# Performance work log

Hardware: AMD Instinct MI355X
Metric: run time of the kernel (lower is better)

The kernel has to match this reference:

```python
import jax, jax.numpy as jnp
import numpy as np

B, H, S, DK, DV = 2, 16, 2048, 64, 64


def setup_inputs() -> dict:
    key = jax.random.key(0)
    kq, kk, kv = jax.random.split(key, 3)
    queries = jax.random.normal(kq, (B, H, S, DK), dtype=jnp.float32)
    keys = jax.random.normal(kk, (B, H, S, DK), dtype=jnp.float32)
    values = jax.random.normal(kv, (B, H, S, DV), dtype=jnp.float32)
    # causal boolean mask, broadcastable over batch and heads
    mask = jnp.tril(jnp.ones((S, S), dtype=bool))[None, None, :, :]
    return {"queries": queries, "keys": keys, "values": values, "d_k": DK, "mask": mask}


def reference(queries, keys, values, d_k, mask):
    scale = 1.0 / jnp.sqrt(jnp.float32(d_k))
    # scores: [B, H, S, S]
    scores = jnp.einsum("bhqd,bhkd->bhqk", queries, keys) * scale
    mask_f = mask.astype(jnp.float32)
    scores = scores + (-1e9) * (1.0 - mask_f)
    weights = jax.nn.softmax(scores, axis=-1)
    # second mask step from the original: min(|mask|, |weights|)
    weights = jnp.minimum(jnp.abs(mask_f), jnp.abs(weights))
    return jnp.einsum("bhqk,bhkd->bhqd", weights, values)
```

## Files before the change

kernel.cpp:

```cpp
#include <hip/hip_runtime.h>
#include <hip/hip_bf16.h>

#define B_ 2
#define H_ 16
#define S_ 2048
#define D_ 64

typedef __attribute__((ext_vector_type(8))) short bf16x8;
typedef __attribute__((ext_vector_type(8))) unsigned short u16x8;
typedef __attribute__((ext_vector_type(4))) unsigned int u32x4;
typedef __attribute__((ext_vector_type(4))) float f32x4;
typedef unsigned short ushort_t;

#define SCALE 0.18033688011112042f
#define MFIX 12.0f

__device__ __forceinline__ unsigned short f2bf(float x) {
  unsigned int u = __builtin_bit_cast(unsigned int, x);
  unsigned int r = (u + 0x7FFFu + ((u >> 16) & 1u)) >> 16;
  return (unsigned short)r;
}

__device__ __forceinline__ unsigned int cvt_pk_bf16(float lo, float hi) {
  unsigned int r;
  asm("v_cvt_pk_bf16_f32 %0, %1, %2" : "=v"(r) : "v"(lo), "v"(hi));
  return r;
}

__device__ __forceinline__ float fast_exp2(float x) {
  float r;
  asm("v_exp_f32 %0, %1" : "=v"(r) : "v"(x));
  return r;
}

__device__ __forceinline__ int sigma_row(int rl) {
  return (rl & 0x23) | ((rl & 0x0C) << 1) | ((rl & 0x10) >> 2);
}

#define GLL16(gp, lp)                                                          \
  __builtin_amdgcn_global_load_lds(                                            \
      (const __attribute__((address_space(1))) unsigned int*)(gp),             \
      (__attribute__((address_space(3))) unsigned int*)(lp), 16, 0, 0)

__global__ void prepack(const float* __restrict__ Kf, const float* __restrict__ Vf,
                        ushort_t* __restrict__ Kg, ushort_t* __restrict__ Vtg) {
  const int blk = blockIdx.x;
  const int tid = threadIdx.x;
  const int bh = blk >> 5, t = blk & 31;
  const float* srcK = Kf + ((size_t)bh * S_ + (size_t)t * 64) * D_;
  const float* srcV = Vf + ((size_t)bh * S_ + (size_t)t * 64) * D_;
  ushort_t* dK = Kg + (size_t)blk * 4096;
  ushort_t* dV = Vtg + (size_t)blk * 4096;
  for (int is = 0; is < 2; ++is) {
    const int e = is * 2048 + tid * 8;
    {
      const int rl = e >> 6, pos = (e >> 3) & 7, ch = pos ^ (rl & 7);
      const float* sp = srcK + sigma_row(rl) * 64 + ch * 8;
      float4 a = *(const float4*)sp;
      float4 b = *(const float4*)(sp + 4);
      u16x8 w;
      w[0] = f2bf(a.x); w[1] = f2bf(a.y); w[2] = f2bf(a.z); w[3] = f2bf(a.w);
      w[4] = f2bf(b.x); w[5] = f2bf(b.y); w[6] = f2bf(b.z); w[7] = f2bf(b.w);
      *(u16x8*)(dK + e) = w;
    }
    {
      const int d0 = e >> 6, pos = (e >> 3) & 7, ch = pos ^ (d0 & 7);
      u16x8 w;
      for (int i = 0; i < 8; ++i) w[i] = f2bf(srcV[(size_t)(ch * 8 + i) * 64 + d0]);
      *(u16x8*)(dV + e) = w;
    }
  }
}

__launch_bounds__(256, 5)
__global__ void attn_split(const float* __restrict__ Qf, const ushort_t* __restrict__ Kg,
                           const ushort_t* __restrict__ Vtg, float* __restrict__ O,
                           float* __restrict__ PO, float* __restrict__ ML) {
  const int bh = blockIdx.x;
  const int y = blockIdx.y;
  int qt, c;
  if (y == 0) { qt = 15; c = 0; }
  else if (y <= 16) { qt = 15 + y; c = 0; }
  else if (y == 17) { qt = 31; c = 1; }
  else { const int p = y - 18, k = 15 - (p >> 1);
         if (p & 1) { qt = k + 15; c = 1; } else { qt = k - 1; c = 0; } }
  const int t0 = c << 4;
  const int t1 = (qt < t0 + 15) ? qt : (t0 + 15);

  const int tid = threadIdx.x;
  const int wave = tid >> 6, lane = tid & 63;
  const int col = lane & 15, g = lane >> 4;

  __shared__ __align__(16) ushort_t Kl[2][64][64];
  __shared__ __align__(16) ushort_t Vt[2][64][64];

  const int qrow = qt * 64 + wave * 16 + col;
  bf16x8 qf[2];
  {
    const float* Qh = Qf + (size_t)bh * S_ * D_;
    for (int kk = 0; kk < 2; ++kk) {
      const float* p = Qh + (size_t)qrow * 64 + kk * 32 + g * 8;
      float4 a = *(const float4*)p;
      float4 b = *(const float4*)(p + 4);
      float v[8] = {a.x, a.y, a.z, a.w, b.x, b.y, b.z, b.w};
      bf16x8 w;
      for (int i = 0; i < 8; ++i) w[i] = (short)f2bf(v[i] * SCALE);
      qf[kk] = w;
    }
  }

  f32x4 acc[4] = {};
  float l_ = 0.0f;

  const int ch0 = (g ^ (col & 7)) << 3;
  const int ch1 = ((4 | g) ^ (col & 7)) << 3;

  auto STAGE = [&](int t, int b) {
    const ushort_t* kg = Kg + ((size_t)(bh * 32 + t)) * 4096;
    const ushort_t* vg = Vtg + ((size_t)(bh * 32 + t)) * 4096;
    GLL16(kg + tid * 8,        &Kl[b][0][0] + tid * 8);
    GLL16(kg + 2048 + tid * 8, &Kl[b][0][0] + 2048 + tid * 8);
    GLL16(vg + tid * 8,        &Vt[b][0][0] + tid * 8);
    GLL16(vg + 2048 + tid * 8, &Vt[b][0][0] + 2048 + tid * 8);
  };

  auto COMPUTE = [&](int b, bool diag) {
    const f32x4 cinit = {-MFIX, -MFIX, -MFIX, -MFIX};
    f32x4 s[4] = {cinit, cinit, cinit, cinit};
    __builtin_amdgcn_s_setprio(1);
    #pragma unroll
    for (int nt = 0; nt < 4; ++nt) {
      const ushort_t* row = &Kl[b][nt * 16 + col][0];
      const bf16x8 kf0 = *(const bf16x8*)(row + ch0);
      const bf16x8 kf1 = *(const bf16x8*)(row + ch1);
      s[nt] = __builtin_amdgcn_mfma_f32_16x16x32_bf16(kf0, qf[0], s[nt], 0, 0, 0);
      s[nt] = __builtin_amdgcn_mfma_f32_16x16x32_bf16(kf1, qf[1], s[nt], 0, 0, 0);
    }
    __builtin_amdgcn_s_setprio(0);
    if (diag) {
      const int qloc = wave * 16 + col;
      #pragma unroll
      for (int nt = 0; nt < 4; ++nt) {
        const int tau_base = 32 * (nt >> 1) + 4 * (nt & 1) + 8 * g;
        #pragma unroll
        for (int r = 0; r < 4; ++r)
          if (tau_base + r > qloc) s[nt][r] = -INFINITY;
      }
    }
    #pragma unroll
    for (int nt = 0; nt < 4; ++nt)
      #pragma unroll
      for (int r = 0; r < 4; ++r) s[nt][r] = fast_exp2(s[nt][r]);
    const float b0 = (s[0][0] + s[0][1]) + (s[0][2] + s[0][3]);
    const float b1 = (s[1][0] + s[1][1]) + (s[1][2] + s[1][3]);
    const float b2 = (s[2][0] + s[2][1]) + (s[2][2] + s[2][3]);
    const float b3 = (s[3][0] + s[3][1]) + (s[3][2] + s[3][3]);
    l_ += (b0 + b1) + (b2 + b3);
    u32x4 w0, w1;
    w0[0] = cvt_pk_bf16(s[0][0], s[0][1]); w0[1] = cvt_pk_bf16(s[0][2], s[0][3]);
    w0[2] = cvt_pk_bf16(s[1][0], s[1][1]); w0[3] = cvt_pk_bf16(s[1][2], s[1][3]);
    w1[0] = cvt_pk_bf16(s[2][0], s[2][1]); w1[1] = cvt_pk_bf16(s[2][2], s[2][3]);
    w1[2] = cvt_pk_bf16(s[3][0], s[3][1]); w1[3] = cvt_pk_bf16(s[3][2], s[3][3]);
    const bf16x8 pf0 = __builtin_bit_cast(bf16x8, w0);
    const bf16x8 pf1 = __builtin_bit_cast(bf16x8, w1);
    __builtin_amdgcn_s_setprio(1);
    #pragma unroll
    for (int nt = 0; nt < 4; ++nt) {
      const ushort_t* row = &Vt[b][nt * 16 + col][0];
      const bf16x8 vf0 = *(const bf16x8*)(row + ch0);
      const bf16x8 vf1 = *(const bf16x8*)(row + ch1);
      acc[nt] = __builtin_amdgcn_mfma_f32_16x16x32_bf16(vf0, pf0, acc[nt], 0, 0, 0);
      acc[nt] = __builtin_amdgcn_mfma_f32_16x16x32_bf16(vf1, pf1, acc[nt], 0, 0, 0);
    }
    __builtin_amdgcn_s_setprio(0);
  };

  int cur = 0;
  STAGE(t0, 0);
  __syncthreads();
  for (int t = t0; t <= t1; ++t) {
    if (t < t1) STAGE(t + 1, cur ^ 1);
    COMPUTE(cur, t == qt);
    __syncthreads();
    cur ^= 1;
  }

  float lsum = l_;
  lsum += __shfl_xor(lsum, 16);
  lsum += __shfl_xor(lsum, 32);
  const int rowloc = wave * 16 + col;
  if (qt <= 15) {
    const float inv = 1.0f / lsum;
    float* dst = O + (size_t)bh * S_ * D_ + (size_t)qrow * 64;
    #pragma unroll
    for (int nt = 0; nt < 4; ++nt) {
      f32x4 v = acc[nt];
      v *= inv;
      *(f32x4*)(dst + nt * 16 + 4 * g) = v;
    }
  } else {
    float* po = PO + (size_t)((((bh << 4) + (qt - 16)) << 1) + c) * 4096;
    #pragma unroll
    for (int nt = 0; nt < 4; ++nt)
      *(f32x4*)(po + rowloc * 64 + nt * 16 + 4 * g) = acc[nt];
    if (g == 0)
      ML[(size_t)((((bh << 4) + (qt - 16)) << 1) + c) * 64 + rowloc] = lsum;
  }
}

__global__ void merge_partials(const float* __restrict__ PO, const float* __restrict__ ML,
                               float* __restrict__ O) {
  const int bh = blockIdx.x;
  const int q16 = blockIdx.y;
  const int tid = threadIdx.x;
  const int r = tid >> 2, d0 = (tid & 3) << 4;
  const size_t base = (size_t)((bh << 4) + q16) << 1;
  const float l0 = ML[base * 64 + r];
  const float l1 = ML[(base + 1) * 64 + r];
  const float inv = 1.0f / (l0 + l1);
  const float* p0 = PO + base * 4096 + r * 64 + d0;
  const float* p1 = PO + (base + 1) * 4096 + r * 64 + d0;
  float* out = O + ((size_t)bh * S_ + (size_t)(16 + q16) * 64 + r) * 64 + d0;
  #pragma unroll
  for (int j = 0; j < 4; ++j) {
    float4 x = *(const float4*)(p0 + 4 * j);
    float4 y = *(const float4*)(p1 + 4 * j);
    float4 o;
    o.x = (x.x + y.x) * inv; o.y = (x.y + y.y) * inv;
    o.z = (x.z + y.z) * inv; o.w = (x.w + y.w) * inv;
    *(float4*)(out + 4 * j) = o;
  }
}

__launch_bounds__(256, 4)
__global__ void attn_fb(const float* __restrict__ Qf, const float* __restrict__ Kf,
                        const float* __restrict__ Vf, float* __restrict__ O) {
  const int bh = blockIdx.x;
  const int qt = 31 - blockIdx.y;
  const int tid = threadIdx.x;
  const int wave = tid >> 6, lane = tid & 63;
  const int col = lane & 15, g = lane >> 4;
  __shared__ __align__(16) ushort_t Kl[2][64][64];
  __shared__ __align__(16) ushort_t Vt[2][64][64];
  const int qrow = qt * 64 + wave * 16 + col;
  bf16x8 qf[2];
  {
    const float* Qh = Qf + (size_t)bh * S_ * D_;
    for (int kk = 0; kk < 2; ++kk) {
      const float* pp = Qh + (size_t)qrow * 64 + kk * 32 + g * 8;
      float4 a = *(const float4*)pp;
      float4 b = *(const float4*)(pp + 4);
      float v[8] = {a.x, a.y, a.z, a.w, b.x, b.y, b.z, b.w};
      bf16x8 w;
      for (int i = 0; i < 8; ++i) w[i] = (short)f2bf(v[i] * SCALE);
      qf[kk] = w;
    }
  }
  f32x4 acc[4] = {};
  float l_ = 0.0f;
  const int ch0 = (g ^ (col & 7)) << 3;
  const int ch1 = ((4 | g) ^ (col & 7)) << 3;
  auto STAGE = [&](int t, int b) {
    const float* Kh = Kf + (size_t)bh * S_ * D_;
    const float* Vh = Vf + (size_t)bh * S_ * D_;
    {
      const int rl = tid >> 2;
      const int c0 = (tid & 3) << 4;
      const float* src = Kh + ((size_t)(t * 64 + sigma_row(rl))) * 64 + c0;
      for (int jj = 0; jj < 2; ++jj) {
        float4 x = *(const float4*)(src + jj * 8);
        float4 yv = *(const float4*)(src + jj * 8 + 4);
        u16x8 w;
        w[0] = f2bf(x.x); w[1] = f2bf(x.y); w[2] = f2bf(x.z); w[3] = f2bf(x.w);
        w[4] = f2bf(yv.x); w[5] = f2bf(yv.y); w[6] = f2bf(yv.z); w[7] = f2bf(yv.w);
        const int ch = (c0 >> 3) + jj;
        *(u16x8*)&Kl[b][rl][(ch ^ (rl & 7)) << 3] = w;
      }
    }
    {
      const int cc = tid & 63;
      const int r0 = (tid >> 6) << 4;
      const float* src = Vh + ((size_t)(t * 64 + r0)) * 64 + cc;
      for (int jj = 0; jj < 2; ++jj) {
        u16x8 w;
        for (int i = 0; i < 8; ++i) w[i] = f2bf(src[(size_t)(jj * 8 + i) * 64]);
        const int ch = (r0 >> 3) + jj;
        *(u16x8*)&Vt[b][cc][(ch ^ (cc & 7)) << 3] = w;
      }
    }
  };
  auto COMPUTE = [&](int b, bool diag) {
    const f32x4 cinit = {-MFIX, -MFIX, -MFIX, -MFIX};
    f32x4 s[4] = {cinit, cinit, cinit, cinit};
    for (int nt = 0; nt < 4; ++nt) {
      const ushort_t* row = &Kl[b][nt * 16 + col][0];
      const bf16x8 kf0 = *(const bf16x8*)(row + ch0);
      const bf16x8 kf1 = *(const bf16x8*)(row + ch1);
      s[nt] = __builtin_amdgcn_mfma_f32_16x16x32_bf16(kf0, qf[0], s[nt], 0, 0, 0);
      s[nt] = __builtin_amdgcn_mfma_f32_16x16x32_bf16(kf1, qf[1], s[nt], 0, 0, 0);
    }
    if (diag) {
      const int qloc = wave * 16 + col;
      for (int nt = 0; nt < 4; ++nt) {
        const int tb = 32 * (nt >> 1) + 4 * (nt & 1) + 8 * g;
        for (int r = 0; r < 4; ++r)
          if (tb + r > qloc) s[nt][r] = -INFINITY;
      }
    }
    float sum = 0.0f;
    for (int nt = 0; nt < 4; ++nt)
      for (int r = 0; r < 4; ++r) {
        const float pv = fast_exp2(s[nt][r]);
        s[nt][r] = pv;
        sum += pv;
      }
    l_ += sum;
    u32x4 t0, t1;
    t0[0] = cvt_pk_bf16(s[0][0], s[0][1]); t0[1] = cvt_pk_bf16(s[0][2], s[0][3]);
    t0[2] = cvt_pk_bf16(s[1][0], s[1][1]); t0[3] = cvt_pk_bf16(s[1][2], s[1][3]);
    t1[0] = cvt_pk_bf16(s[2][0], s[2][1]); t1[1] = cvt_pk_bf16(s[2][2], s[2][3]);
    t1[2] = cvt_pk_bf16(s[3][0], s[3][1]); t1[3] = cvt_pk_bf16(s[3][2], s[3][3]);
    const bf16x8 pf0 = __builtin_bit_cast(bf16x8, t0);
    const bf16x8 pf1 = __builtin_bit_cast(bf16x8, t1);
    for (int nt = 0; nt < 4; ++nt) {
      const ushort_t* row = &Vt[b][nt * 16 + col][0];
      const bf16x8 vf0 = *(const bf16x8*)(row + ch0);
      const bf16x8 vf1 = *(const bf16x8*)(row + ch1);
      acc[nt] = __builtin_amdgcn_mfma_f32_16x16x32_bf16(vf0, pf0, acc[nt], 0, 0, 0);
      acc[nt] = __builtin_amdgcn_mfma_f32_16x16x32_bf16(vf1, pf1, acc[nt], 0, 0, 0);
    }
  };
  int cur = 0;
  STAGE(0, 0);
  __syncthreads();
  for (int t = 0; t <= qt; ++t) {
    if (t < qt) STAGE(t + 1, cur ^ 1);
    COMPUTE(cur, t == qt);
    __syncthreads();
    cur ^= 1;
  }
  float lsum = l_;
  lsum += __shfl_xor(lsum, 16);
  lsum += __shfl_xor(lsum, 32);
  const float inv = 1.0f / lsum;
  float* dst = O + (size_t)bh * S_ * D_ + (size_t)qrow * 64;
  for (int nt = 0; nt < 4; ++nt) {
    f32x4 v = acc[nt];
    v *= inv;
    *(f32x4*)(dst + nt * 16 + 4 * g) = v;
  }
}

extern "C" void kernel_launch(void* const* d_in, const int* in_sizes, int n_in,
                              void* d_out, int out_size, void* d_ws, size_t ws_size,
                              hipStream_t stream) {
  const float* Q = (const float*)d_in[0];
  const float* K = (const float*)d_in[1];
  const float* V = (const float*)d_in[2];
  float* O = (float*)d_out;
  const size_t NE = (size_t)B_ * H_ * S_ * D_;
  const size_t needK = 2 * NE * sizeof(ushort_t);
  const size_t PO_elems = 32ull * 16 * 2 * 4096;
  const size_t ML_elems = 32ull * 16 * 2 * 64;
  const size_t needSplit = needK + (PO_elems + ML_elems) * sizeof(float);
  if (ws_size >= needSplit) {
    ushort_t* kg = (ushort_t*)d_ws;
    float* PO = (float*)((char*)d_ws + needK);
    float* ML = PO + PO_elems;
    prepack<<<1024, 256, 0, stream>>>(K, V, kg, kg + NE);
    attn_split<<<dim3(32, 48), 256, 0, stream>>>(Q, kg, kg + NE, O, PO, ML);
    merge_partials<<<dim3(32, 16), 256, 0, stream>>>(PO, ML, O);
  } else {
    attn_fb<<<dim3(32, 32), 256, 0, stream>>>(Q, K, V, O);
  }
}
```

Before: 52.21 us.

## Use 128-row query blocks with 8-wave workgroups sharing each K/V tile

Each workgroup now has 8 waves covering two 64-row query tiles, so every K/V tile staged in shared memory serves 128 query rows instead of 64. The work split and partial-merge layout are redone for 128-row blocks, giving 24 blocks per head instead of 48. Waves whose query tile ends before the current key tile skip the compute but still join the barriers. The goal is to halve K/V staging traffic per query row, at the cost of idle waves on diagonal tiles and fewer, larger workgroups.

```diff
diff --git a/kernel.cpp b/kernel.cpp
--- a/kernel.cpp
+++ b/kernel.cpp
@@ -72,29 +72,30 @@
   }
 }
 
-__launch_bounds__(256, 5)
-__global__ void attn_split(const float* __restrict__ Qf, const ushort_t* __restrict__ Kg,
-                           const ushort_t* __restrict__ Vtg, float* __restrict__ O,
-                           float* __restrict__ PO, float* __restrict__ ML) {
+__launch_bounds__(512, 8)
+__global__ void attn8w(const float* __restrict__ Qf, const ushort_t* __restrict__ Kg,
+                       const ushort_t* __restrict__ Vtg, float* __restrict__ O,
+                       float* __restrict__ PO, float* __restrict__ ML) {
   const int bh = blockIdx.x;
   const int y = blockIdx.y;
-  int qt, c;
-  if (y == 0) { qt = 15; c = 0; }
-  else if (y <= 16) { qt = 15 + y; c = 0; }
-  else if (y == 17) { qt = 31; c = 1; }
-  else { const int p = y - 18, k = 15 - (p >> 1);
-         if (p & 1) { qt = k + 15; c = 1; } else { qt = k - 1; c = 0; } }
-  const int t0 = c << 4;
-  const int t1 = (qt < t0 + 15) ? qt : (t0 + 15);
+  int qb, c, t0, t1;
+  if (y < 8) { qb = 8 + y; c = 0; t0 = 0; t1 = 15; }
+  else {
+    const int k = y - 8, pair = k >> 1;
+    if ((k & 1) == 0) { qb = 15 - pair; c = 1; t0 = 16; t1 = 2 * qb + 1; }
+    else              { qb = 7 - pair;  c = 0; t0 = 0;  t1 = 2 * qb + 1; }
+  }
 
   const int tid = threadIdx.x;
   const int wave = tid >> 6, lane = tid & 63;
   const int col = lane & 15, g = lane >> 4;
+  const int myqt = 2 * qb + (wave >> 2);
+  const int qloc = (wave & 3) * 16 + col;
 
   __shared__ __align__(16) ushort_t Kl[2][64][64];
   __shared__ __align__(16) ushort_t Vt[2][64][64];
 
-  const int qrow = qt * 64 + wave * 16 + col;
+  const int qrow = qb * 128 + wave * 16 + col;
   bf16x8 qf[2];
   {
     const float* Qh = Qf + (size_t)bh * S_ * D_;
@@ -118,10 +119,8 @@
   auto STAGE = [&](int t, int b) {
     const ushort_t* kg = Kg + ((size_t)(bh * 32 + t)) * 4096;
     const ushort_t* vg = Vtg + ((size_t)(bh * 32 + t)) * 4096;
-    GLL16(kg + tid * 8,        &Kl[b][0][0] + tid * 8);
-    GLL16(kg + 2048 + tid * 8, &Kl[b][0][0] + 2048 + tid * 8);
-    GLL16(vg + tid * 8,        &Vt[b][0][0] + tid * 8);
-    GLL16(vg + 2048 + tid * 8, &Vt[b][0][0] + 2048 + tid * 8);
+    GLL16(kg + tid * 8, &Kl[b][0][0] + tid * 8);
+    GLL16(vg + tid * 8, &Vt[b][0][0] + tid * 8);
   };
 
   auto COMPUTE = [&](int b, bool diag) {
@@ -138,7 +137,6 @@
     }
     __builtin_amdgcn_s_setprio(0);
     if (diag) {
-      const int qloc = wave * 16 + col;
       #pragma unroll
       for (int nt = 0; nt < 4; ++nt) {
         const int tau_base = 32 * (nt >> 1) + 4 * (nt & 1) + 8 * g;
@@ -180,7 +178,7 @@
   __syncthreads();
   for (int t = t0; t <= t1; ++t) {
     if (t < t1) STAGE(t + 1, cur ^ 1);
-    COMPUTE(cur, t == qt);
+    if (t <= myqt) COMPUTE(cur, t == myqt);
     __syncthreads();
     cur ^= 1;
   }
@@ -189,7 +187,7 @@
   lsum += __shfl_xor(lsum, 16);
   lsum += __shfl_xor(lsum, 32);
   const int rowloc = wave * 16 + col;
-  if (qt <= 15) {
+  if (qb < 8) {
     const float inv = 1.0f / lsum;
     float* dst = O + (size_t)bh * S_ * D_ + (size_t)qrow * 64;
     #pragma unroll
@@ -199,35 +197,35 @@
       *(f32x4*)(dst + nt * 16 + 4 * g) = v;
     }
   } else {
-    float* po = PO + (size_t)((((bh << 4) + (qt - 16)) << 1) + c) * 4096;
+    const int slot = ((bh << 3) + (qb - 8)) * 2 + c;
+    float* po = PO + (size_t)slot * 8192;
     #pragma unroll
     for (int nt = 0; nt < 4; ++nt)
       *(f32x4*)(po + rowloc * 64 + nt * 16 + 4 * g) = acc[nt];
-    if (g == 0)
-      ML[(size_t)((((bh << 4) + (qt - 16)) << 1) + c) * 64 + rowloc] = lsum;
+    if (g == 0) ML[(size_t)slot * 128 + rowloc] = lsum;
   }
 }
 
 __global__ void merge_partials(const float* __restrict__ PO, const float* __restrict__ ML,
                                float* __restrict__ O) {
   const int bh = blockIdx.x;
-  const int q16 = blockIdx.y;
+  const int q8 = blockIdx.y;
   const int tid = threadIdx.x;
   const int r = tid >> 2, d0 = (tid & 3) << 4;
-  const size_t base = (size_t)((bh << 4) + q16) << 1;
-  const float l0 = ML[base * 64 + r];
-  const float l1 = ML[(base + 1) * 64 + r];
+  const int slot = ((bh << 3) + q8) * 2;
+  const float l0 = ML[(size_t)slot * 128 + r];
+  const float l1 = ML[(size_t)(slot + 1) * 128 + r];
   const float inv = 1.0f / (l0 + l1);
-  const float* p0 = PO + base * 4096 + r * 64 + d0;
-  const float* p1 = PO + (base + 1) * 4096 + r * 64 + d0;
-  float* out = O + ((size_t)bh * S_ + (size_t)(16 + q16) * 64 + r) * 64 + d0;
+  const float* p0 = PO + (size_t)slot * 8192 + r * 64 + d0;
+  const float* p1 = PO + (size_t)(slot + 1) * 8192 + r * 64 + d0;
+  float* out = O + ((size_t)bh * S_ + (size_t)(8 + q8) * 128 + r) * 64 + d0;
   #pragma unroll
   for (int j = 0; j < 4; ++j) {
     float4 x = *(const float4*)(p0 + 4 * j);
-    float4 y = *(const float4*)(p1 + 4 * j);
+    float4 yv = *(const float4*)(p1 + 4 * j);
     float4 o;
-    o.x = (x.x + y.x) * inv; o.y = (x.y + y.y) * inv;
-    o.z = (x.z + y.z) * inv; o.w = (x.w + y.w) * inv;
+    o.x = (x.x + yv.x) * inv; o.y = (x.y + yv.y) * inv;
+    o.z = (x.z + yv.z) * inv; o.w = (x.w + yv.w) * inv;
     *(float4*)(out + 4 * j) = o;
   }
 }
@@ -360,16 +358,16 @@
   float* O = (float*)d_out;
   const size_t NE = (size_t)B_ * H_ * S_ * D_;
   const size_t needK = 2 * NE * sizeof(ushort_t);
-  const size_t PO_elems = 32ull * 16 * 2 * 4096;
-  const size_t ML_elems = 32ull * 16 * 2 * 64;
+  const size_t PO_elems = 32ull * 8 * 2 * 8192;
+  const size_t ML_elems = 32ull * 8 * 2 * 128;
   const size_t needSplit = needK + (PO_elems + ML_elems) * sizeof(float);
   if (ws_size >= needSplit) {
     ushort_t* kg = (ushort_t*)d_ws;
     float* PO = (float*)((char*)d_ws + needK);
     float* ML = PO + PO_elems;
     prepack<<<1024, 256, 0, stream>>>(K, V, kg, kg + NE);
-    attn_split<<<dim3(32, 48), 256, 0, stream>>>(Q, kg, kg + NE, O, PO, ML);
-    merge_partials<<<dim3(32, 16), 256, 0, stream>>>(PO, ML, O);
+    attn8w<<<dim3(32, 24), 512, 0, stream>>>(Q, kg, kg + NE, O, PO, ML);
+    merge_partials<<<dim3(32, 8), 512, 0, stream>>>(PO, ML, O);
   } else {
     attn_fb<<<dim3(32, 32), 256, 0, stream>>>(Q, K, V, O);
   }
```

New measurement: 50.95 us, median of 3. -2.4%, faster.
